# Kernel optimization log

Measured on AMD Instinct MI355X. Metric: run time of the kernel, lower is better.

The kernel has to match this reference:

```python
import jax, jax.numpy as jnp
import numpy as np

# Module config (matches init_kwargs)
H, W, C = 32, 32, 256
K = 3                      # filter_size
B = 16
TEMP = 1.0                 # softmax_temp
CH, CW = H - K + 1, W - K + 1   # convs_height/width (valid padding, stride 1)
NF = CH * CW               # num_convs
FS = K * K                 # filter_size squared (window size)
HW = H * W


def _local_indices():
    # flattened (row-major over H,W) positions of each KxK window, sorted ascending
    idx = np.zeros((NF, FS), dtype=np.int32)
    c = 0
    for i in range(CH):
        for j in range(CW):
            win = [(i + di) * W + (j + dj) for di in range(K) for dj in range(K)]
            idx[c] = np.sort(win)
            c += 1
    return jnp.asarray(idx)


def setup_inputs() -> dict:
    key = jax.random.key(0)
    ks = jax.random.split(key, 7)
    s = 1.0 / np.sqrt(C)  # torch Linear default init scale
    return {
        "batch": jax.random.normal(ks[0], (B, C, H, W), dtype=jnp.float32),
        "key_w": jax.random.uniform(ks[1], (C, C), jnp.float32, -s, s),
        "key_b": jax.random.uniform(ks[2], (C,), jnp.float32, -s, s),
        "query_w": jax.random.uniform(ks[3], (C, C), jnp.float32, -s, s),
        "query_b": jax.random.uniform(ks[4], (C,), jnp.float32, -s, s),
        "value_w": jax.random.uniform(ks[5], (1, C), jnp.float32, -s, s),
        "value_b": jax.random.uniform(ks[6], (1,), jnp.float32, -s, s),
        "local_indices": _local_indices(),
    }


def _normalize(t):
    # F.normalize(dim=-1), eps=1e-12
    return t / jnp.maximum(jnp.linalg.norm(t, axis=-1, keepdims=True), 1e-12)


def reference(batch, key_w, key_b, query_w, query_b, value_w, value_b, local_indices):
    # [B,C,H,W] -> [B,HW,C]
    x = batch.transpose(0, 2, 3, 1).reshape(B, HW, C)
    # local patches: X_l[f,b,k,c] = x[b, local_indices[f,k], c]  -> [NF,B,FS,C]
    X_l = x[:, local_indices].transpose(1, 0, 2, 3)
    # global is the full (unmasked) feature map: X_g = x  -> [B,HW,C]
    keys = x @ key_w.T + key_b                       # [B,HW,C]
    queries = X_l @ query_w.T + query_b              # [NF,B,FS,C]
    values = (x @ value_w.T + value_b)[..., 0]       # [B,HW]
    # cosine similarity: [NF,B,HW,FS]
    comp = jnp.einsum('bnc,fbkc->fbnk', _normalize(keys), _normalize(queries))
    att = jax.nn.softmax(TEMP * comp, axis=2)        # softmax over HW
    # W_g[f,b,k] = sum_n values[b,n] * att[f,b,n,k]
    W_g = jnp.einsum('bn,fbnk->fbk', values, att)
    # convolved: sum over window positions, weighted
    conv = jnp.einsum('fbk,fbkc->fbc', W_g, X_l)     # [NF,B,C]
    out = conv.transpose(1, 0, 2).reshape(B, CH, CW, C).transpose(0, 3, 1, 2)
    return out  # [B,C,CH,CW]
```

## Files before the change

kernel.cpp:

```cpp
#include <hip/hip_runtime.h>
#include <hip/hip_bf16.h>


#define NB 16
#define NC 256
#define NHW 1024
#define NCH 30

typedef __attribute__((ext_vector_type(8))) short short8;
typedef __attribute__((ext_vector_type(4))) float f32x4;

static __device__ __forceinline__ unsigned short f2bf(float f) {
    __hip_bfloat16 h = __float2bfloat16(f);
    return *(unsigned short*)&h;
}
static __device__ __forceinline__ float bf2f(unsigned short u) {
    unsigned int x = ((unsigned int)u) << 16;
    return __uint_as_float(x);
}

__global__ __launch_bounds__(256) void wconv_kernel(
    const float* __restrict__ key_w, const float* __restrict__ query_w,
    unsigned short* __restrict__ kpk, unsigned short* __restrict__ qpk)
{
    const int gx = blockIdx.x;
    const int mat = gx >> 3, g = gx & 7, t = threadIdx.x;
    const float* src = mat ? query_w : key_w;
    unsigned short* dst = mat ? qpk : kpk;
    #pragma unroll
    for (int it = 0; it < 4; ++it) {
        int idx = it * 256 + t;
        int ct = idx >> 6, lane = idx & 63;
        int l15 = lane & 15, q = lane >> 4;
        const float* s = src + (ct * 16 + l15) * NC + g * 32 + q * 8;
        float4 a = *(const float4*)s;
        float4 c = *(const float4*)(s + 4);
        short8 o;
        o[0] = (short)f2bf(a.x); o[1] = (short)f2bf(a.y);
        o[2] = (short)f2bf(a.z); o[3] = (short)f2bf(a.w);
        o[4] = (short)f2bf(c.x); o[5] = (short)f2bf(c.y);
        o[6] = (short)f2bf(c.z); o[7] = (short)f2bf(c.w);
        *(short8*)(dst + ((size_t)(g * 16 + ct) * 64 + lane) * 8) = o;
    }
}

__global__ __launch_bounds__(256, 3) void fused_lin_kernel(
    const float* __restrict__ batch,
    const float* __restrict__ value_w, const float* __restrict__ value_b,
    const unsigned short* __restrict__ kpk, const unsigned short* __restrict__ qpk,
    const float* __restrict__ key_b, const float* __restrict__ query_b,
    unsigned short* __restrict__ xc,
    unsigned short* __restrict__ Kn, unsigned short* __restrict__ Qn,
    float* __restrict__ vout)
{
    const int b = blockIdx.y, n0 = blockIdx.x * 16;
    const int t = threadIdx.x, wave = t >> 6, lane = t & 63;
    const int l15 = lane & 15, quad = lane >> 4;

    __shared__ unsigned short Xs[2][16][72];
    __shared__ float PK[4][16], PQ[4][16];
    __shared__ float4 vred[4][4];

    const int c_l = t >> 2;
    const int n4  = (t & 3) * 4;
    const float* bb = batch + (size_t)b * NC * NHW + n0;
    unsigned short* xcp = xc + (size_t)b * NC * NHW + n0;
    float4 vacc = {0.f, 0.f, 0.f, 0.f};

    const unsigned short* kbase = kpk + (size_t)(wave * 4) * 512 + lane * 8;
    const unsigned short* qbase = qpk + (size_t)(wave * 4) * 512 + lane * 8;

    short8 wK[2][4], wQ[2][4];
    #pragma unroll
    for (int ct = 0; ct < 4; ++ct) {
        wK[0][ct] = *(const short8*)(kbase + ct * 512);
        wQ[0][ct] = *(const short8*)(qbase + ct * 512);
    }

    {
        float4 x0 = *(const float4*)(bb + (size_t)c_l * NHW + n4);
        ushort4 o0;
        o0.x = f2bf(x0.x); o0.y = f2bf(x0.y); o0.z = f2bf(x0.z); o0.w = f2bf(x0.w);
        *(ushort4*)(xcp + (size_t)c_l * NHW + n4) = o0;
        float w0 = value_w[c_l];
        vacc.x += x0.x * w0; vacc.y += x0.y * w0;
        vacc.z += x0.z * w0; vacc.w += x0.w * w0;
        Xs[0][n4 + 0][c_l] = o0.x; Xs[0][n4 + 1][c_l] = o0.y;
        Xs[0][n4 + 2][c_l] = o0.z; Xs[0][n4 + 3][c_l] = o0.w;
    }
    __syncthreads();

    f32x4 accK[4], accQ[4];
    #pragma unroll
    for (int ct = 0; ct < 4; ++ct) {
        int co = wave * 64 + ct * 16 + l15;
        float bK = key_b[co], bQ = query_b[co];
        accK[ct] = (f32x4){bK, bK, bK, bK};
        accQ[ct] = (f32x4){bQ, bQ, bQ, bQ};
    }

    for (int cc = 0; cc < 4; ++cc) {
        float4 x_pf;
        if (cc < 3)
            x_pf = *(const float4*)(bb + (size_t)((cc + 1) * 64 + c_l) * NHW + n4);

        const int cur = cc & 1;
        #pragma unroll
        for (int kc = 0; kc < 2; ++kc) {
            const int g = cc * 2 + kc;
            if (g < 7) {
                const int nb_ = (g + 1) & 1;
                #pragma unroll
                for (int ct = 0; ct < 4; ++ct) {
                    wK[nb_][ct] = *(const short8*)(kbase + (g + 1) * 8192 + ct * 512);
                    wQ[nb_][ct] = *(const short8*)(qbase + (g + 1) * 8192 + ct * 512);
                }
            }
            short8 af = *(const short8*)&Xs[cur][l15][kc * 32 + quad * 8];
            const int cb = g & 1;
            #pragma unroll
            for (int ct = 0; ct < 4; ++ct) {
                accK[ct] = __builtin_amdgcn_mfma_f32_16x16x32_bf16(af, wK[cb][ct], accK[ct], 0, 0, 0);
                accQ[ct] = __builtin_amdgcn_mfma_f32_16x16x32_bf16(af, wQ[cb][ct], accQ[ct], 0, 0, 0);
            }
        }

        if (cc < 3) {
            int c0 = (cc + 1) * 64 + c_l;
            ushort4 o0;
            o0.x = f2bf(x_pf.x); o0.y = f2bf(x_pf.y);
            o0.z = f2bf(x_pf.z); o0.w = f2bf(x_pf.w);
            *(ushort4*)(xcp + (size_t)c0 * NHW + n4) = o0;
            float w0 = value_w[c0];
            vacc.x += x_pf.x * w0; vacc.y += x_pf.y * w0;
            vacc.z += x_pf.z * w0; vacc.w += x_pf.w * w0;
            const int nxt = (cc + 1) & 1;
            Xs[nxt][n4 + 0][c_l] = o0.x; Xs[nxt][n4 + 1][c_l] = o0.y;
            Xs[nxt][n4 + 2][c_l] = o0.z; Xs[nxt][n4 + 3][c_l] = o0.w;
            __syncthreads();
        }
    }

    vacc.x += __shfl_xor(vacc.x, 4, 64); vacc.x += __shfl_xor(vacc.x, 8, 64);
    vacc.x += __shfl_xor(vacc.x, 16, 64); vacc.x += __shfl_xor(vacc.x, 32, 64);
    vacc.y += __shfl_xor(vacc.y, 4, 64); vacc.y += __shfl_xor(vacc.y, 8, 64);
    vacc.y += __shfl_xor(vacc.y, 16, 64); vacc.y += __shfl_xor(vacc.y, 32, 64);
    vacc.z += __shfl_xor(vacc.z, 4, 64); vacc.z += __shfl_xor(vacc.z, 8, 64);
    vacc.z += __shfl_xor(vacc.z, 16, 64); vacc.z += __shfl_xor(vacc.z, 32, 64);
    vacc.w += __shfl_xor(vacc.w, 4, 64); vacc.w += __shfl_xor(vacc.w, 8, 64);
    vacc.w += __shfl_xor(vacc.w, 16, 64); vacc.w += __shfl_xor(vacc.w, 32, 64);

    float nK[4] = {0, 0, 0, 0}, nQ[4] = {0, 0, 0, 0};
    #pragma unroll
    for (int ct = 0; ct < 4; ++ct)
        #pragma unroll
        for (int r = 0; r < 4; ++r) {
            nK[r] += accK[ct][r] * accK[ct][r];
            nQ[r] += accQ[ct][r] * accQ[ct][r];
        }
    #pragma unroll
    for (int r = 0; r < 4; ++r)
        #pragma unroll
        for (int o = 1; o < 16; o <<= 1) {
            nK[r] += __shfl_xor(nK[r], o, 64);
            nQ[r] += __shfl_xor(nQ[r], o, 64);
        }
    if (l15 == 0)
        #pragma unroll
        for (int r = 0; r < 4; ++r) {
            PK[wave][quad * 4 + r] = nK[r];
            PQ[wave][quad * 4 + r] = nQ[r];
        }
    if (lane < 4) vred[wave][lane] = vacc;
    __syncthreads();

    float ik[4], iq[4];
    #pragma unroll
    for (int r = 0; r < 4; ++r) {
        int qr = quad * 4 + r;
        float sk = PK[0][qr] + PK[1][qr] + PK[2][qr] + PK[3][qr];
        float sq = PQ[0][qr] + PQ[1][qr] + PQ[2][qr] + PQ[3][qr];
        ik[r] = 1.f / fmaxf(sqrtf(sk), 1e-12f);
        iq[r] = 1.f / fmaxf(sqrtf(sq), 1e-12f);
    }
    #pragma unroll
    for (int ct = 0; ct < 4; ++ct)
        #pragma unroll
        for (int r = 0; r < 4; ++r) {
            size_t row = (size_t)(b * NHW + n0 + quad * 4 + r) * NC
                       + wave * 64 + ct * 16 + l15;
            Kn[row] = f2bf(accK[ct][r] * ik[r]);
            Qn[row] = f2bf(accQ[ct][r] * iq[r]);
        }
    if (t < 4) {
        float4 s = {0.f, 0.f, 0.f, 0.f};
        #pragma unroll
        for (int w = 0; w < 4; ++w) {
            float4 p = vred[w][t];
            s.x += p.x; s.y += p.y; s.z += p.z; s.w += p.w;
        }
        float vb = value_b[0];
        s.x += vb; s.y += vb; s.z += vb; s.w += vb;
        *(float4*)(vout + b * NHW + n0 + t * 4) = s;
    }
}

__global__ __launch_bounds__(512) void attn_kernel(
    const unsigned short* __restrict__ Kn,
    const unsigned short* __restrict__ Qn,
    const float* __restrict__ vbuf,
    float* __restrict__ R)
{
    const int b = blockIdx.y, m0 = blockIdx.x * 64;
    const int t = threadIdx.x, wave = t >> 6, lane = t & 63;
    const int l15 = lane & 15, quad = lane >> 4;

    short8 bf[4][8];
    #pragma unroll
    for (int ms = 0; ms < 4; ++ms) {
        const short* q = (const short*)Qn
                       + (size_t)(b * NHW + m0 + ms * 16 + l15) * NC + quad * 8;
        #pragma unroll
        for (int c = 0; c < 8; ++c) bf[ms][c] = *(const short8*)(q + 32 * c);
    }
    const float* vb = vbuf + b * NHW;
    const int nstart = wave * 128;
    const short* ka = (const short*)Kn + (size_t)(b * NHW + nstart + l15) * NC + quad * 8;

    float z[4] = {0.f, 0.f, 0.f, 0.f}, tc[4] = {0.f, 0.f, 0.f, 0.f};
    for (int it = 0; it < 8; ++it, ka += 16 * NC) {
        short8 af[8];
        #pragma unroll
        for (int c = 0; c < 8; ++c) af[c] = *(const short8*)(ka + 32 * c);
        f32x4 a0[4], a1[4];
        #pragma unroll
        for (int ms = 0; ms < 4; ++ms) { a0[ms] = (f32x4){0,0,0,0}; a1[ms] = (f32x4){0,0,0,0}; }
        #pragma unroll
        for (int c = 0; c < 4; ++c)
            #pragma unroll
            for (int ms = 0; ms < 4; ++ms) {
                a0[ms] = __builtin_amdgcn_mfma_f32_16x16x32_bf16(af[c],     bf[ms][c],     a0[ms], 0, 0, 0);
                a1[ms] = __builtin_amdgcn_mfma_f32_16x16x32_bf16(af[c + 4], bf[ms][c + 4], a1[ms], 0, 0, 0);
            }
        float4 vv = *(const float4*)(vb + nstart + it * 16 + quad * 4);
        #pragma unroll
        for (int ms = 0; ms < 4; ++ms)
            #pragma unroll
            for (int r = 0; r < 4; ++r) {
                float e = __expf(a0[ms][r] + a1[ms][r]);
                z[ms] += e;
                tc[ms] += ((const float*)&vv)[r] * e;
            }
    }
    #pragma unroll
    for (int ms = 0; ms < 4; ++ms) {
        z[ms]  += __shfl_xor(z[ms], 16, 64);  z[ms]  += __shfl_xor(z[ms], 32, 64);
        tc[ms] += __shfl_xor(tc[ms], 16, 64); tc[ms] += __shfl_xor(tc[ms], 32, 64);
    }

    __shared__ float zs[8][4][16], ts[8][4][16];
    if (lane < 16)
        #pragma unroll
        for (int ms = 0; ms < 4; ++ms) {
            zs[wave][ms][l15] = z[ms];
            ts[wave][ms][l15] = tc[ms];
        }
    __syncthreads();
    if (t < 64) {
        int ms = t >> 4, li = t & 15;
        float zz = 0.f, tt = 0.f;
        #pragma unroll
        for (int w = 0; w < 8; ++w) { zz += zs[w][ms][li]; tt += ts[w][ms][li]; }
        R[b * NHW + m0 + ms * 16 + li] = tt / zz;
    }
}

__global__ __launch_bounds__(256) void out_kernel(
    const unsigned short* __restrict__ xc,
    const float* __restrict__ R,
    float* __restrict__ out)
{
    const int bc = blockIdx.x;
    const int b  = bc >> 8;
    const int t  = threadIdx.x;
    __shared__ float P[NHW];

    const unsigned short* xp = xc + (size_t)bc * NHW;
    const float* rp = R + b * NHW;
    {
        ushort4 xv = *(const ushort4*)(xp + t * 4);
        float4  rv = *(const float4*)(rp + t * 4);
        P[t * 4 + 0] = rv.x * bf2f(xv.x);
        P[t * 4 + 1] = rv.y * bf2f(xv.y);
        P[t * 4 + 2] = rv.z * bf2f(xv.z);
        P[t * 4 + 3] = rv.w * bf2f(xv.w);
    }
    __syncthreads();
    for (int idx = t; idx < NCH * NCH; idx += 256) {
        int i = idx / NCH, j = idx - i * NCH;
        const float* pr = &P[i * 32 + j];
        float s = pr[0]  + pr[1]  + pr[2]
                + pr[32] + pr[33] + pr[34]
                + pr[64] + pr[65] + pr[66];
        out[(size_t)bc * (NCH * NCH) + idx] = s;
    }
}

extern "C" void kernel_launch(void* const* d_in, const int* in_sizes, int n_in,
                              void* d_out, int out_size, void* d_ws, size_t ws_size,
                              hipStream_t stream) {
    const float* batch   = (const float*)d_in[0];
    const float* key_w   = (const float*)d_in[1];
    const float* key_b   = (const float*)d_in[2];
    const float* query_w = (const float*)d_in[3];
    const float* query_b = (const float*)d_in[4];
    const float* value_w = (const float*)d_in[5];
    const float* value_b = (const float*)d_in[6];
    float* out = (float*)d_out;

    char* ws = (char*)d_ws;
    const size_t KQ = (size_t)NB * NHW * NC;
    unsigned short* xc  = (unsigned short*)ws;
    unsigned short* Kn  = xc + KQ;
    unsigned short* Qn  = Kn + KQ;
    unsigned short* kpk = Qn + KQ;
    unsigned short* qpk = kpk + NC * NC;
    float* vbuf = (float*)(qpk + NC * NC);
    float* Rbuf = vbuf + NB * NHW;

    wconv_kernel<<<16, 256, 0, stream>>>(key_w, query_w, kpk, qpk);
    fused_lin_kernel<<<dim3(64, NB), 256, 0, stream>>>(batch, value_w, value_b,
                                                       kpk, qpk, key_b, query_b,
                                                       xc, Kn, Qn, vbuf);
    attn_kernel<<<dim3(16, NB), 512, 0, stream>>>(Kn, Qn, vbuf, Rbuf);
    out_kernel<<<NB * NC, 256, 0, stream>>>(xc, Rbuf, out);
}
```

Baseline: 129.3 us.

## Widen fused linear kernel tile to 32 positions with 8 waves

```diff
diff --git a/kernel.cpp b/kernel.cpp
--- a/kernel.cpp
+++ b/kernel.cpp
@@ -44,7 +44,7 @@
     }
 }
 
-__global__ __launch_bounds__(256, 3) void fused_lin_kernel(
+__global__ __launch_bounds__(512, 3) void fused_lin_kernel(
     const float* __restrict__ batch,
     const float* __restrict__ value_w, const float* __restrict__ value_b,
     const unsigned short* __restrict__ kpk, const unsigned short* __restrict__ qpk,
@@ -53,26 +53,26 @@
     unsigned short* __restrict__ Kn, unsigned short* __restrict__ Qn,
     float* __restrict__ vout)
 {
-    const int b = blockIdx.y, n0 = blockIdx.x * 16;
+    const int b = blockIdx.y, n0 = blockIdx.x * 32;
     const int t = threadIdx.x, wave = t >> 6, lane = t & 63;
     const int l15 = lane & 15, quad = lane >> 4;
 
-    __shared__ unsigned short Xs[2][16][72];
-    __shared__ float PK[4][16], PQ[4][16];
-    __shared__ float4 vred[4][4];
-
-    const int c_l = t >> 2;
-    const int n4  = (t & 3) * 4;
+    __shared__ unsigned short Xs[2][32][72];
+    __shared__ float PK[8][2][16], PQ[8][2][16];
+    __shared__ float4 vred[8][8];
+
+    const int c_l = t >> 3;
+    const int n4  = (t & 7) * 4;
     const float* bb = batch + (size_t)b * NC * NHW + n0;
     unsigned short* xcp = xc + (size_t)b * NC * NHW + n0;
     float4 vacc = {0.f, 0.f, 0.f, 0.f};
 
-    const unsigned short* kbase = kpk + (size_t)(wave * 4) * 512 + lane * 8;
-    const unsigned short* qbase = qpk + (size_t)(wave * 4) * 512 + lane * 8;
-
-    short8 wK[2][4], wQ[2][4];
-    #pragma unroll
-    for (int ct = 0; ct < 4; ++ct) {
+    const unsigned short* kbase = kpk + (size_t)(wave * 2) * 512 + lane * 8;
+    const unsigned short* qbase = qpk + (size_t)(wave * 2) * 512 + lane * 8;
+
+    short8 wK[2][2], wQ[2][2];
+    #pragma unroll
+    for (int ct = 0; ct < 2; ++ct) {
         wK[0][ct] = *(const short8*)(kbase + ct * 512);
         wQ[0][ct] = *(const short8*)(qbase + ct * 512);
     }
@@ -90,13 +90,15 @@
     }
     __syncthreads();
 
-    f32x4 accK[4], accQ[4];
-    #pragma unroll
-    for (int ct = 0; ct < 4; ++ct) {
-        int co = wave * 64 + ct * 16 + l15;
+    f32x4 accK[2][2], accQ[2][2];
+    #pragma unroll
+    for (int ct = 0; ct < 2; ++ct) {
+        int co = wave * 32 + ct * 16 + l15;
         float bK = key_b[co], bQ = query_b[co];
-        accK[ct] = (f32x4){bK, bK, bK, bK};
-        accQ[ct] = (f32x4){bQ, bQ, bQ, bQ};
+        accK[0][ct] = (f32x4){bK, bK, bK, bK};
+        accK[1][ct] = (f32x4){bK, bK, bK, bK};
+        accQ[0][ct] = (f32x4){bQ, bQ, bQ, bQ};
+        accQ[1][ct] = (f32x4){bQ, bQ, bQ, bQ};
     }
 
     for (int cc = 0; cc < 4; ++cc) {
@@ -111,17 +113,20 @@
             if (g < 7) {
                 const int nb_ = (g + 1) & 1;
                 #pragma unroll
-                for (int ct = 0; ct < 4; ++ct) {
+                for (int ct = 0; ct < 2; ++ct) {
                     wK[nb_][ct] = *(const short8*)(kbase + (g + 1) * 8192 + ct * 512);
                     wQ[nb_][ct] = *(const short8*)(qbase + (g + 1) * 8192 + ct * 512);
                 }
             }
-            short8 af = *(const short8*)&Xs[cur][l15][kc * 32 + quad * 8];
+            short8 af0 = *(const short8*)&Xs[cur][l15][kc * 32 + quad * 8];
+            short8 af1 = *(const short8*)&Xs[cur][16 + l15][kc * 32 + quad * 8];
             const int cb = g & 1;
             #pragma unroll
-            for (int ct = 0; ct < 4; ++ct) {
-                accK[ct] = __builtin_amdgcn_mfma_f32_16x16x32_bf16(af, wK[cb][ct], accK[ct], 0, 0, 0);
-                accQ[ct] = __builtin_amdgcn_mfma_f32_16x16x32_bf16(af, wQ[cb][ct], accQ[ct], 0, 0, 0);
+            for (int ct = 0; ct < 2; ++ct) {
+                accK[0][ct] = __builtin_amdgcn_mfma_f32_16x16x32_bf16(af0, wK[cb][ct], accK[0][ct], 0, 0, 0);
+                accK[1][ct] = __builtin_amdgcn_mfma_f32_16x16x32_bf16(af1, wK[cb][ct], accK[1][ct], 0, 0, 0);
+                accQ[0][ct] = __builtin_amdgcn_mfma_f32_16x16x32_bf16(af0, wQ[cb][ct], accQ[0][ct], 0, 0, 0);
+                accQ[1][ct] = __builtin_amdgcn_mfma_f32_16x16x32_bf16(af1, wQ[cb][ct], accQ[1][ct], 0, 0, 0);
             }
         }
 
@@ -141,61 +146,70 @@
         }
     }
 
-    vacc.x += __shfl_xor(vacc.x, 4, 64); vacc.x += __shfl_xor(vacc.x, 8, 64);
-    vacc.x += __shfl_xor(vacc.x, 16, 64); vacc.x += __shfl_xor(vacc.x, 32, 64);
-    vacc.y += __shfl_xor(vacc.y, 4, 64); vacc.y += __shfl_xor(vacc.y, 8, 64);
-    vacc.y += __shfl_xor(vacc.y, 16, 64); vacc.y += __shfl_xor(vacc.y, 32, 64);
-    vacc.z += __shfl_xor(vacc.z, 4, 64); vacc.z += __shfl_xor(vacc.z, 8, 64);
-    vacc.z += __shfl_xor(vacc.z, 16, 64); vacc.z += __shfl_xor(vacc.z, 32, 64);
-    vacc.w += __shfl_xor(vacc.w, 4, 64); vacc.w += __shfl_xor(vacc.w, 8, 64);
-    vacc.w += __shfl_xor(vacc.w, 16, 64); vacc.w += __shfl_xor(vacc.w, 32, 64);
-
-    float nK[4] = {0, 0, 0, 0}, nQ[4] = {0, 0, 0, 0};
-    #pragma unroll
-    for (int ct = 0; ct < 4; ++ct)
+    #pragma unroll
+    for (int o = 8; o <= 32; o <<= 1) {
+        vacc.x += __shfl_xor(vacc.x, o, 64); vacc.y += __shfl_xor(vacc.y, o, 64);
+        vacc.z += __shfl_xor(vacc.z, o, 64); vacc.w += __shfl_xor(vacc.w, o, 64);
+    }
+
+    float nK[2][4] = {{0, 0, 0, 0}, {0, 0, 0, 0}};
+    float nQ[2][4] = {{0, 0, 0, 0}, {0, 0, 0, 0}};
+    #pragma unroll
+    for (int ns = 0; ns < 2; ++ns)
+        #pragma unroll
+        for (int ct = 0; ct < 2; ++ct)
+            #pragma unroll
+            for (int r = 0; r < 4; ++r) {
+                nK[ns][r] += accK[ns][ct][r] * accK[ns][ct][r];
+                nQ[ns][r] += accQ[ns][ct][r] * accQ[ns][ct][r];
+            }
+    #pragma unroll
+    for (int ns = 0; ns < 2; ++ns)
+        #pragma unroll
+        for (int r = 0; r < 4; ++r)
+            #pragma unroll
+            for (int o = 1; o < 16; o <<= 1) {
+                nK[ns][r] += __shfl_xor(nK[ns][r], o, 64);
+                nQ[ns][r] += __shfl_xor(nQ[ns][r], o, 64);
+            }
+    if (l15 == 0)
+        #pragma unroll
+        for (int ns = 0; ns < 2; ++ns)
+            #pragma unroll
+            for (int r = 0; r < 4; ++r) {
+                PK[wave][ns][quad * 4 + r] = nK[ns][r];
+                PQ[wave][ns][quad * 4 + r] = nQ[ns][r];
+            }
+    if (lane < 8) vred[wave][lane] = vacc;
+    __syncthreads();
+
+    float ik[2][4], iq[2][4];
+    #pragma unroll
+    for (int ns = 0; ns < 2; ++ns)
         #pragma unroll
         for (int r = 0; r < 4; ++r) {
-            nK[r] += accK[ct][r] * accK[ct][r];
-            nQ[r] += accQ[ct][r] * accQ[ct][r];
-        }
-    #pragma unroll
-    for (int r = 0; r < 4; ++r)
-        #pragma unroll
-        for (int o = 1; o < 16; o <<= 1) {
-            nK[r] += __shfl_xor(nK[r], o, 64);
-            nQ[r] += __shfl_xor(nQ[r], o, 64);
-        }
-    if (l15 == 0)
-        #pragma unroll
-        for (int r = 0; r < 4; ++r) {
-            PK[wave][quad * 4 + r] = nK[r];
-            PQ[wave][quad * 4 + r] = nQ[r];
-        }
-    if (lane < 4) vred[wave][lane] = vacc;
-    __syncthreads();
-
-    float ik[4], iq[4];
-    #pragma unroll
-    for (int r = 0; r < 4; ++r) {
-        int qr = quad * 4 + r;
-        float sk = PK[0][qr] + PK[1][qr] + PK[2][qr] + PK[3][qr];
-        float sq = PQ[0][qr] + PQ[1][qr] + PQ[2][qr] + PQ[3][qr];
-        ik[r] = 1.f / fmaxf(sqrtf(sk), 1e-12f);
-        iq[r] = 1.f / fmaxf(sqrtf(sq), 1e-12f);
-    }
-    #pragma unroll
-    for (int ct = 0; ct < 4; ++ct)
-        #pragma unroll
-        for (int r = 0; r < 4; ++r) {
-            size_t row = (size_t)(b * NHW + n0 + quad * 4 + r) * NC
-                       + wave * 64 + ct * 16 + l15;
-            Kn[row] = f2bf(accK[ct][r] * ik[r]);
-            Qn[row] = f2bf(accQ[ct][r] * iq[r]);
-        }
-    if (t < 4) {
+            int qr = quad * 4 + r;
+            float sk = 0.f, sq = 0.f;
+            #pragma unroll
+            for (int w = 0; w < 8; ++w) { sk += PK[w][ns][qr]; sq += PQ[w][ns][qr]; }
+            ik[ns][r] = 1.f / fmaxf(sqrtf(sk), 1e-12f);
+            iq[ns][r] = 1.f / fmaxf(sqrtf(sq), 1e-12f);
+        }
+    #pragma unroll
+    for (int ns = 0; ns < 2; ++ns)
+        #pragma unroll
+        for (int ct = 0; ct < 2; ++ct)
+            #pragma unroll
+            for (int r = 0; r < 4; ++r) {
+                size_t row = (size_t)(b * NHW + n0 + ns * 16 + quad * 4 + r) * NC
+                           + wave * 32 + ct * 16 + l15;
+                Kn[row] = f2bf(accK[ns][ct][r] * ik[ns][r]);
+                Qn[row] = f2bf(accQ[ns][ct][r] * iq[ns][r]);
+            }
+    if (t < 8) {
         float4 s = {0.f, 0.f, 0.f, 0.f};
         #pragma unroll
-        for (int w = 0; w < 4; ++w) {
+        for (int w = 0; w < 8; ++w) {
             float4 p = vred[w][t];
             s.x += p.x; s.y += p.y; s.z += p.z; s.w += p.w;
         }
@@ -329,7 +343,7 @@
     float* Rbuf = vbuf + NB * NHW;
 
     wconv_kernel<<<16, 256, 0, stream>>>(key_w, query_w, kpk, qpk);
-    fused_lin_kernel<<<dim3(64, NB), 256, 0, stream>>>(batch, value_w, value_b,
+    fused_lin_kernel<<<dim3(32, NB), 512, 0, stream>>>(batch, value_w, value_b,
                                                        kpk, qpk, key_b, query_b,
                                                        xc, Kn, Qn, vbuf);
     attn_kernel<<<dim3(16, NB), 512, 0, stream>>>(Kn, Qn, vbuf, Rbuf);
```

After: 127.5 us. No clear change (-1.4%).
